# Performance work log

Hardware: AMD Instinct MI355X
Metric: run time of the kernel (lower is better)

The kernel has to match this reference:

```python
import jax, jax.numpy as jnp
import numpy as np

NEG_SLOPE = 0.2
EPS = 1e-16


def sp_gat_layer(h, src, trg, w, a_src, a_trg):
    # h: [N, f_in], w: [H, f_in, f_out], a_src/a_trg: [H, f_out]
    n = h.shape[0]
    h_prime = jnp.einsum('nf,hfo->nho', h, w)            # [N, H, O]
    attn_src = jnp.einsum('nho,ho->nh', h_prime, a_src)  # [N, H]
    attn_trg = jnp.einsum('nho,ho->nh', h_prime, a_trg)  # [N, H]
    e = jax.nn.leaky_relu(attn_src[src] + attn_trg[trg], NEG_SLOPE)  # [E, H]
    e = e - e.max()  # global max-shift, as in the torch code
    exp_e = jnp.exp(e)
    denom = jax.ops.segment_sum(exp_e, trg, num_segments=n)          # [N, H]
    neigh_attn = exp_e / (denom[trg] + EPS)                          # [E, H]
    h_weighted = h_prime[src] * neigh_attn[..., None]                # [E, H, O]
    return jax.ops.segment_sum(h_weighted, trg, num_segments=n)     # [N, H, O]


def run_stack(h, src, trg, params):
    # params: list of (w, a_src, a_trg); last layer mean over heads, others elu+flatten
    n = h.shape[0]
    n_layers = len(params)
    for i, (w, a_src, a_trg) in enumerate(params):
        out = sp_gat_layer(h, src, trg, w, a_src, a_trg)  # [N, H, O]
        if i + 1 == n_layers:
            h = out.mean(axis=1)                          # [N, O]
        else:
            h = jax.nn.elu(out.reshape(n, -1))            # [N, H*O]
    return h


def setup_inputs() -> dict:
    key = jax.random.key(0)
    ks = jax.random.split(key, 24)
    N, E = 60000, 800000
    H, F0, O = 8, 128, 32
    inp = {
        'h0': jax.random.normal(ks[0], (N, F0), jnp.float32),
        'h1': jax.random.normal(ks[1], (N, F0), jnp.float32),
        'src0': jax.random.randint(ks[2], (E,), 0, N),
        'trg0': jax.random.randint(ks[3], (E,), 0, N),
        'src1': jax.random.randint(ks[4], (E,), 0, N),
        'trg1': jax.random.randint(ks[5], (E,), 0, N),
        'w00': jax.random.normal(ks[6], (H, F0, O), jnp.float32) * 0.1,
        'asrc00': jax.random.normal(ks[7], (H, O), jnp.float32) * 0.1,
        'atrg00': jax.random.normal(ks[8], (H, O), jnp.float32) * 0.1,
        'w01': jax.random.normal(ks[9], (H, H * O, O), jnp.float32) * 0.1,
        'asrc01': jax.random.normal(ks[10], (H, O), jnp.float32) * 0.1,
        'atrg01': jax.random.normal(ks[11], (H, O), jnp.float32) * 0.1,
        'w10': jax.random.normal(ks[12], (H, F0, O), jnp.float32) * 0.1,
        'asrc10': jax.random.normal(ks[13], (H, O), jnp.float32) * 0.1,
        'atrg10': jax.random.normal(ks[14], (H, O), jnp.float32) * 0.1,
        'w11': jax.random.normal(ks[15], (H, H * O, O), jnp.float32) * 0.1,
        'asrc11': jax.random.normal(ks[16], (H, O), jnp.float32) * 0.1,
        'atrg11': jax.random.normal(ks[17], (H, O), jnp.float32) * 0.1,
        'fc_w': jax.random.normal(ks[18], (2 * O, 2), jnp.float32) * 0.1,
        'fc_b': jnp.zeros((2,), jnp.float32),
    }
    return inp


N_USER = 50000


def reference(h0, h1, src0, trg0, src1, trg1,
              w00, asrc00, atrg00, w01, asrc01, atrg01,
              w10, asrc10, atrg10, w11, asrc11, atrg11,
              fc_w, fc_b):
    emb0 = run_stack(h0, src0, trg0, [(w00, asrc00, atrg00), (w01, asrc01, atrg01)])
    emb1 = run_stack(h1, src1, trg1, [(w10, asrc10, atrg10), (w11, asrc11, atrg11)])
    ret = jnp.concatenate([emb0[:N_USER], emb1[:N_USER]], axis=-1)  # [n_user, 64]
    logits = ret @ fc_w + fc_b
    return jax.nn.log_softmax(logits, axis=-1)
```

## Files before the change

### kernel.cpp

```cpp
#include <hip/hip_runtime.h>
#include <math.h>

#define H 8
#define O 32
#define C 256
#define CAP 48
#define NEG_SLOPE 0.2f
#define EPS_V 1e-16f
#define LOG2E 1.4426950408889634f

#define W_BKT 128
#define NB_PAD 512
#define BCAP 2048
#define EPB 4096

typedef float f32x4 __attribute__((ext_vector_type(4)));
typedef float f32x2 __attribute__((ext_vector_type(2)));
typedef short bf16x8 __attribute__((ext_vector_type(8)));

__device__ __forceinline__ unsigned short f2bf(float x){
  unsigned u = __float_as_uint(x);
  unsigned r = (u + 0x7fffu + ((u >> 16) & 1u)) >> 16;
  return (unsigned short)r;
}

template<int F>
__device__ __forceinline__ void cvt_w_body(const float* __restrict__ w,
                                           short* __restrict__ wb, int t){
  constexpr int KB = F / 8;
  if (t >= 256 * KB) return;
  int c = t & 255, kb = t >> 8;
  int h = c >> 5, o = c & 31;
  bf16x8 out;
  for (int j = 0; j < 8; ++j){
    int f = kb * 8 + j;
    out[j] = (short)f2bf(w[((size_t)h * F + f) * O + o]);
  }
  *(bf16x8*)(wb + ((size_t)kb * 256 + c) * 8) = out;
}

__device__ void pass1_body(const int* __restrict__ trg, const int* __restrict__ src,
                           unsigned* __restrict__ gbuf, unsigned* __restrict__ gcur,
                           int E, int bx, int tid){
  __shared__ int cnt[NB_PAD];
  __shared__ int offl[NB_PAD];
  __shared__ unsigned baseg[NB_PAD];
  __shared__ int cur[NB_PAD];
  __shared__ unsigned payload[EPB];

  const int e0 = bx * EPB;
  const int ne = min(EPB, E - e0);
  for (int i = tid; i < NB_PAD; i += 256) cnt[i] = 0;
  __syncthreads();
  for (int i = tid; i < ne; i += 256){
    int t = trg[e0 + i];
    atomicAdd(&cnt[t >> 7], 1);
  }
  __syncthreads();
  for (int i = tid; i < NB_PAD; i += 256){
    int c = cnt[i];
    baseg[i] = c ? atomicAdd(&gcur[i], (unsigned)c) : 0u;
  }
  if (tid < 64){
    int v[8]; int s = 0;
#pragma unroll
    for (int j = 0; j < 8; ++j){ v[j] = cnt[tid * 8 + j]; s += v[j]; }
    int x = s;
#pragma unroll
    for (int d = 1; d < 64; d <<= 1){
      int o = __shfl_up(x, d, 64);
      if (tid >= d) x += o;
    }
    int base = x - s;
#pragma unroll
    for (int j = 0; j < 8; ++j){ offl[tid * 8 + j] = base; base += v[j]; }
  }
  __syncthreads();
  for (int i = tid; i < NB_PAD; i += 256) cur[i] = offl[i];
  __syncthreads();
  for (int i = tid; i < ne; i += 256){
    int t = trg[e0 + i];
    int s = src[e0 + i];
    int b = t >> 7;
    int p = atomicAdd(&cur[b], 1);
    payload[p] = ((unsigned)b << 23) | ((unsigned)(t & 127) << 16) | (unsigned)s;
  }
  __syncthreads();
  for (int i = tid; i < ne; i += 256){
    unsigned v = payload[i];
    unsigned b = v >> 23;
    unsigned pos = baseg[b] + (unsigned)(i - offl[b]);
    if (pos < BCAP) gbuf[(size_t)b * BCAP + pos] = v;
  }
}

__device__ void pass2_body(const unsigned* __restrict__ gbuf,
                           const unsigned* __restrict__ gcur,
                           unsigned short* __restrict__ csrc, int* __restrict__ degv,
                           int N, int bx, int tid){
  __shared__ unsigned short ell[W_BKT * CAP];
  __shared__ int dcnt[W_BKT];
  const int node0 = bx << 7;
  const int nn = min(W_BKT, N - node0);
  const unsigned pat = ((unsigned)N << 16) | (unsigned)N;
  unsigned* e32 = (unsigned*)ell;
  for (int i = tid; i < W_BKT * CAP / 2; i += 256) e32[i] = pat;
  for (int i = tid; i < W_BKT; i += 256) dcnt[i] = 0;
  __syncthreads();
  const int ne = min((int)gcur[bx], BCAP);
  for (int i = tid; i < ne; i += 256){
    unsigned v = gbuf[(size_t)bx * BCAP + i];
    int lt = (v >> 16) & 127;
    int p = atomicAdd(&dcnt[lt], 1);
    if (p < CAP) ell[lt * CAP + p] = (unsigned short)(v & 0xffffu);
  }
  __syncthreads();
  const uint4* s4 = (const uint4*)ell;
  uint4* d4 = (uint4*)(csrc + (size_t)node0 * CAP);
  const int n16 = nn * (CAP / 8);
  for (int i = tid; i < n16; i += 256) d4[i] = s4[i];
  for (int i = tid; i < nn; i += 256) degv[node0 + i] = dcnt[i];
}

__device__ __forceinline__ float gather_accum(
    const unsigned char* __restrict__ hp,
    const float* __restrict__ as_, float ath,
    const unsigned short* __restrict__ row, int deg, int l, int head,
    f32x2 (&acc)[4]){
  int degR = (deg + 7) & ~7;
  float dsum = 0.f;
  for (int jb = 0; jb < degR; jb += 8){
    ushort4 s4a = *(const ushort4*)(row + jb);
    ushort4 s4b = *(const ushort4*)(row + jb + 4);
    int ss[8] = {s4a.x, s4a.y, s4a.z, s4a.w, s4b.x, s4b.y, s4b.z, s4b.w};
    float xa[8];
#pragma unroll
    for (int i = 0; i < 8; ++i) xa[i] = as_[ss[i] * H + head];
    uint2 vv[8];
#pragma unroll
    for (int i = 0; i < 8; ++i)
      vv[i] = *(const uint2*)(hp + (size_t)ss[i] * C + l * 8);
#pragma unroll
    for (int i = 0; i < 8; ++i){
      float x = xa[i] + ath;
      x = fmaxf(x, NEG_SLOPE * x);
      float e = __builtin_amdgcn_exp2f(x);
      dsum += e;
      f32x2 ee = {e, e};
      f32x2 u0 = __builtin_amdgcn_cvt_pk_f32_fp8(vv[i].x, false);
      f32x2 u1 = __builtin_amdgcn_cvt_pk_f32_fp8(vv[i].x, true);
      f32x2 u2 = __builtin_amdgcn_cvt_pk_f32_fp8(vv[i].y, false);
      f32x2 u3 = __builtin_amdgcn_cvt_pk_f32_fp8(vv[i].y, true);
      acc[0] += u0 * ee;
      acc[1] += u1 * ee;
      acc[2] += u2 * ee;
      acc[3] += u3 * ee;
    }
  }
  return dsum;
}

__device__ __forceinline__ void gemm_epilogue(
    f32x4 (&acc)[2][4], int node0, int q, int m15, int wv,
    const float* __restrict__ wsv, const float* __restrict__ wtv,
    unsigned char* __restrict__ hpo, float* __restrict__ aso,
    float* __restrict__ ato, int n_nodes){
#pragma unroll
  for (int rt2 = 0; rt2 < 2; ++rt2){
    int nb = node0 + rt2 * 16 + q * 4;
    float att[4][4] = {};
#pragma unroll
    for (int ct = 0; ct < 4; ++ct){
      int col = (wv * 4 + ct) * 16 + m15;
      int hi = ct >> 1;
      int p01 = __builtin_amdgcn_cvt_pk_fp8_f32(acc[rt2][ct][0], acc[rt2][ct][1], 0, false);
      int p23 = __builtin_amdgcn_cvt_pk_fp8_f32(acc[rt2][ct][2], acc[rt2][ct][3], 0, false);
      unsigned char qb[4] = {(unsigned char)(p01 & 0xff),
                             (unsigned char)((p01 >> 8) & 0xff),
                             (unsigned char)(p23 & 0xff),
                             (unsigned char)((p23 >> 8) & 0xff)};
#pragma unroll
      for (int r = 0; r < 4; ++r){
        int n = nb + r;
        if (n < n_nodes) hpo[(size_t)n * C + col] = qb[r];
        float vr = acc[rt2][ct][r];
        att[r][hi]     = fmaf(vr, wsv[ct], att[r][hi]);
        att[r][2 + hi] = fmaf(vr, wtv[ct], att[r][2 + hi]);
      }
    }
#pragma unroll
    for (int r = 0; r < 4; ++r)
#pragma unroll
      for (int k = 0; k < 4; ++k){
        float v = att[r][k];
        v += __shfl_xor(v, 1, 64);
        v += __shfl_xor(v, 2, 64);
        v += __shfl_xor(v, 4, 64);
        v += __shfl_xor(v, 8, 64);
        att[r][k] = v;
      }
    if (m15 == 0){
      int h0i = 2 * wv;
#pragma unroll
      for (int r = 0; r < 4; ++r){
        int n = nb + r;
        if (n < n_nodes){
          aso[n * H + h0i]     = att[r][0] * LOG2E;
          aso[n * H + h0i + 1] = att[r][1] * LOG2E;
          ato[n * H + h0i]     = att[r][2] * LOG2E;
          ato[n * H + h0i + 1] = att[r][3] * LOG2E;
        }
      }
    }
  }
}

__global__ void prep_kernel(
    const float* __restrict__ w000, const float* __restrict__ w100,
    const float* __restrict__ w001, const float* __restrict__ w101,
    const int* __restrict__ t0, const int* __restrict__ t1,
    const int* __restrict__ s0, const int* __restrict__ s1,
    short* __restrict__ wb0, short* __restrict__ wb1,
    unsigned* __restrict__ gbuf, unsigned* __restrict__ gcur,
    float* __restrict__ asA, float* __restrict__ asB,
    int N, int E, int p1B, size_t wbStride, size_t asStride){
  int y = blockIdx.y;
  int bx = blockIdx.x;
  int tid = threadIdx.x;
  if (bx < 16){
    cvt_w_body<128>(y ? w100 : w000, wb0 + (size_t)y * wbStride, bx * 256 + tid);
    return;
  }
  bx -= 16;
  if (bx < 32){
    cvt_w_body<256>(y ? w101 : w001, wb1 + (size_t)y * wbStride, bx * 256 + tid);
    return;
  }
  bx -= 32;
  if (bx < p1B){
    pass1_body(y ? t1 : t0, y ? s1 : s0,
               gbuf + (size_t)y * NB_PAD * BCAP, gcur + (size_t)y * NB_PAD,
               E, bx, tid);
    return;
  }
  if (tid < H){
    asA[y * asStride + (size_t)N * H + tid] = -1e30f;
    asB[y * asStride + (size_t)N * H + tid] = -1e30f;
  }
}

__global__ __launch_bounds__(256) void binfill_gemm0_kernel(
    const unsigned* __restrict__ gbuf, const unsigned* __restrict__ gcur,
    unsigned short* __restrict__ csrc, int* __restrict__ cursor, int N, int NBk,
    const float* __restrict__ h0, const float* __restrict__ h1,
    const short* __restrict__ wb0,
    const float* __restrict__ aps0, const float* __restrict__ apt0,
    const float* __restrict__ aps1, const float* __restrict__ apt1,
    unsigned char* __restrict__ hpA, float* __restrict__ asA, float* __restrict__ atA,
    size_t wbStride, size_t hpStride, size_t asStride){
  __shared__ short atile[32 * 128];
  int y = blockIdx.y;
  int bx = blockIdx.x;
  if (bx < NBk){
    pass2_body(gbuf + (size_t)y * NB_PAD * BCAP, gcur + (size_t)y * NB_PAD,
               csrc + (size_t)y * N * CAP, cursor + (size_t)y * N, N, bx, threadIdx.x);
    return;
  }
  bx -= NBk;
  const float* hsrc = y ? h1 : h0;
  const int tid = threadIdx.x;
  const int node0 = bx * 32;
  {
    int row = tid >> 3, seg = tid & 7;
    int node = node0 + row;
    bf16x8 o0, o1;
    if (node < N){
      const float4* p4 = (const float4*)(hsrc + (size_t)node * 128 + seg * 16);
      float4 p0 = p4[0], p1 = p4[1], p2 = p4[2], p3 = p4[3];
      float v[16] = {p0.x,p0.y,p0.z,p0.w, p1.x,p1.y,p1.z,p1.w,
                     p2.x,p2.y,p2.z,p2.w, p3.x,p3.y,p3.z,p3.w};
#pragma unroll
      for (int j = 0; j < 8; ++j){ o0[j] = (short)f2bf(v[j]); o1[j] = (short)f2bf(v[8+j]); }
    } else {
#pragma unroll
      for (int j = 0; j < 8; ++j){ o0[j] = 0; o1[j] = 0; }
    }
    int key = (row & 7) << 4;
    char* base = (char*)atile + row * 256;
    *(bf16x8*)(base + ((seg * 32) ^ key))      = o0;
    *(bf16x8*)(base + ((seg * 32 + 16) ^ key)) = o1;
  }
  __syncthreads();
  const int wv = tid >> 6, lane = tid & 63;
  const int q = lane >> 4, m15 = lane & 15;
  const float* a_src = y ? aps1 : aps0;
  const float* a_trg = y ? apt1 : apt0;
  float wsv[4], wtv[4];
#pragma unroll
  for (int ct = 0; ct < 4; ++ct){
    int col = (wv * 4 + ct) * 16 + m15;
    wsv[ct] = a_src[col];
    wtv[ct] = a_trg[col];
  }
  const short* wb = wb0 + (size_t)y * wbStride;
  f32x4 acc[2][4] = {};
  const int key = (m15 & 7) << 4;
#pragma unroll
  for (int kk = 0; kk < 4; ++kk){
    const int kb0 = kk * 4 + q;
    bf16x8 a0 = *(const bf16x8*)((char*)atile + m15 * 256 + ((kb0 * 16) ^ key));
    bf16x8 a1 = *(const bf16x8*)((char*)atile + (16 + m15) * 256 + ((kb0 * 16) ^ key));
    const short* wp = wb + ((size_t)kb0 * 256 + wv * 64 + m15) * 8;
#pragma unroll
    for (int ct = 0; ct < 4; ++ct){
      bf16x8 b = *(const bf16x8*)(wp + ct * 128);
      acc[0][ct] = __builtin_amdgcn_mfma_f32_16x16x32_bf16(a0, b, acc[0][ct], 0, 0, 0);
      acc[1][ct] = __builtin_amdgcn_mfma_f32_16x16x32_bf16(a1, b, acc[1][ct], 0, 0, 0);
    }
  }
  gemm_epilogue(acc, node0, q, m15, wv, wsv, wtv,
                hpA + (size_t)y * hpStride, asA + (size_t)y * asStride,
                atA + (size_t)y * asStride, N);
}

__global__ __launch_bounds__(256, 8) void aggmm_kernel(
    const unsigned char* __restrict__ hpA,
    const float* __restrict__ asA, const float* __restrict__ atA,
    const unsigned short* __restrict__ csrc, const int* __restrict__ degv,
    const short* __restrict__ wb1,
    const float* __restrict__ aps0, const float* __restrict__ apt0,
    const float* __restrict__ aps1, const float* __restrict__ apt1,
    unsigned char* __restrict__ hpB, float* __restrict__ asB, float* __restrict__ atB,
    int N, size_t hpStride, size_t asStride, size_t wbStride){
  __shared__ short atile[32 * 256];
  const int y = blockIdx.y;
  const unsigned char* hp = hpA + (size_t)y * hpStride;
  const float* as0_ = asA + (size_t)y * asStride;
  const float* at0_ = atA + (size_t)y * asStride;
  const unsigned short* cs = csrc + (size_t)y * (size_t)N * CAP;
  const int* dg = degv + (size_t)y * N;

  const int tid = threadIdx.x;
  const int wv = tid >> 6, lane = tid & 63, half = lane >> 5, l = lane & 31;
  const int head = l >> 2;
  const int node0 = blockIdx.x * 32;

#pragma unroll
  for (int p = 0; p < 4; ++p){
    int nl = wv * 2 + half + p * 8;
    int node = node0 + nl;
    if (node < N){
      float ath = at0_[node * H + head];
      int deg = dg[node];
      deg = (deg > CAP) ? CAP : deg;
      f32x2 acc[4] = {};
      float dsum = gather_accum(hp, as0_, ath, cs + (size_t)node * CAP, deg, l, head, acc);
      float inv = __builtin_amdgcn_rcpf(dsum + EPS_V);
      bf16x8 o;
#pragma unroll
      for (int k = 0; k < 4; ++k){
        float ax = acc[k].x * inv, ay = acc[k].y * inv;
        float rx = (ax > 0.f) ? ax : (__expf(ax) - 1.f);
        float ry = (ay > 0.f) ? ay : (__expf(ay) - 1.f);
        o[2*k]   = (short)f2bf(rx);
        o[2*k+1] = (short)f2bf(ry);
      }
      *(bf16x8*)((char*)atile + nl * 512 + ((l * 16) ^ ((nl & 7) << 4))) = o;
    }
  }
  __syncthreads();

  const int q = lane >> 4, m15 = lane & 15;
  const float* a_src = y ? aps1 : aps0;
  const float* a_trg = y ? apt1 : apt0;
  float wsv[4], wtv[4];
#pragma unroll
  for (int ct = 0; ct < 4; ++ct){
    int col = (wv * 4 + ct) * 16 + m15;
    wsv[ct] = a_src[col];
    wtv[ct] = a_trg[col];
  }
  const short* wb = wb1 + (size_t)y * wbStride;
  f32x4 acc[2][4] = {};
  const int key = (m15 & 7) << 4;
#pragma unroll
  for (int kk = 0; kk < 8; ++kk){
    const int kb0 = kk * 4 + q;
    bf16x8 a0 = *(const bf16x8*)((char*)atile + m15 * 512 + ((kb0 * 16) ^ key));
    bf16x8 a1 = *(const bf16x8*)((char*)atile + (16 + m15) * 512 + ((kb0 * 16) ^ key));
    const short* wp = wb + ((size_t)kb0 * 256 + wv * 64 + m15) * 8;
#pragma unroll
    for (int ct = 0; ct < 4; ++ct){
      bf16x8 b = *(const bf16x8*)(wp + ct * 128);
      acc[0][ct] = __builtin_amdgcn_mfma_f32_16x16x32_bf16(a0, b, acc[0][ct], 0, 0, 0);
      acc[1][ct] = __builtin_amdgcn_mfma_f32_16x16x32_bf16(a1, b, acc[1][ct], 0, 0, 0);
    }
  }
  gemm_epilogue(acc, node0, q, m15, wv, wsv, wtv,
                hpB + (size_t)y * hpStride, asB + (size_t)y * asStride,
                atB + (size_t)y * asStride, N);
}

__global__ __launch_bounds__(256, 8) void gather_fc_kernel(
    const unsigned char* __restrict__ hpB, size_t hpStride,
    const float* __restrict__ asB, const float* __restrict__ atB, size_t asStride,
    const unsigned short* __restrict__ csrc, const int* __restrict__ degv, int N,
    const float* __restrict__ fw, const float* __restrict__ fb,
    float* __restrict__ out, int n_user){
  int node = (blockIdx.x * 256 + threadIdx.x) >> 6;
  if (node >= n_user) return;
  int lane = threadIdx.x & 63;
  int half = lane >> 5;
  int l = lane & 31;
  int head = l >> 2;
  const unsigned char* hps = hpB + (size_t)half * hpStride;
  const float* ass = asB + (size_t)half * asStride;
  const float* ats = atB + (size_t)half * asStride;
  const unsigned short* row = csrc + (size_t)half * N * CAP + (size_t)node * CAP;
  int deg = degv[(size_t)half * N + node];
  deg = (deg > CAP) ? CAP : deg;
  float ath = ats[node * H + head];
  f32x2 acc[4] = {};
  float dsum = gather_accum(hps, ass, ath, row, deg, l, head, acc);
  float inv = __builtin_amdgcn_rcpf(dsum + EPS_V);
#pragma unroll
  for (int k = 0; k < 4; ++k){ acc[k].x *= inv; acc[k].y *= inv; }
#pragma unroll
  for (int mask = 4; mask <= 16; mask <<= 1){
#pragma unroll
    for (int k = 0; k < 4; ++k){
      acc[k].x += __shfl_xor(acc[k].x, mask, 64);
      acc[k].y += __shfl_xor(acc[k].y, mask, 64);
    }
  }
  float p0 = 0.f, p1 = 0.f;
  if (l < 4){
    float v[8] = {acc[0].x, acc[0].y, acc[1].x, acc[1].y,
                  acc[2].x, acc[2].y, acc[3].x, acc[3].y};
#pragma unroll
    for (int j = 0; j < 8; ++j){
      float e = v[j] * 0.125f;
      int d = half * 32 + l * 8 + j;
      p0 = fmaf(e, fw[d * 2 + 0], p0);
      p1 = fmaf(e, fw[d * 2 + 1], p1);
    }
  }
#pragma unroll
  for (int mask = 1; mask <= 32; mask <<= 1){
    p0 += __shfl_xor(p0, mask, 64);
    p1 += __shfl_xor(p1, mask, 64);
  }
  if (lane == 0){
    float l0 = p0 + fb[0], l1 = p1 + fb[1];
    float m = fmaxf(l0, l1);
    float lse = m + logf(expf(l0 - m) + expf(l1 - m));
    out[(size_t)node * 2 + 0] = l0 - lse;
    out[(size_t)node * 2 + 1] = l1 - lse;
  }
}

extern "C" void kernel_launch(void* const* d_in, const int* in_sizes, int n_in,
                              void* d_out, int out_size, void* d_ws, size_t ws_size,
                              hipStream_t stream){
  const float* h0 = (const float*)d_in[0];
  const float* h1 = (const float*)d_in[1];
  const int* src0 = (const int*)d_in[2];
  const int* trg0 = (const int*)d_in[3];
  const int* src1 = (const int*)d_in[4];
  const int* trg1 = (const int*)d_in[5];
  const float* W [2][2] = {{(const float*)d_in[6],  (const float*)d_in[9]},
                           {(const float*)d_in[12], (const float*)d_in[15]}};
  const float* AS[2][2] = {{(const float*)d_in[7],  (const float*)d_in[10]},
                           {(const float*)d_in[13], (const float*)d_in[16]}};
  const float* AT[2][2] = {{(const float*)d_in[8],  (const float*)d_in[11]},
                           {(const float*)d_in[14], (const float*)d_in[17]}};
  const float* fc_w = (const float*)d_in[18];
  const float* fc_b = (const float*)d_in[19];
  float* out = (float*)d_out;

  const int N = in_sizes[0] / 128;
  const int E = in_sizes[2];
  const int n_user = out_size / 2;

  const size_t HPS = (size_t)(N + 16) * C;
  const size_t WBS = (size_t)32 * 256 * 8;
  const size_t NHP = (size_t)(N + 1) * H;

  float* ws = (float*)d_ws;
  float* attn_sA = ws;  ws += 2 * NHP;
  float* attn_tA = ws;  ws += 2 * NHP;
  float* attn_sB = ws;  ws += 2 * NHP;
  float* attn_tB = ws;  ws += 2 * NHP;
  unsigned char* hpA = (unsigned char*)ws;  ws += 2 * HPS / 4;
  unsigned char* hpB = (unsigned char*)ws;  ws += 2 * HPS / 4;
  short* wb0 = (short*)ws;  ws += 2 * WBS / 2;
  short* wb1 = (short*)ws;  ws += 2 * WBS / 2;
  unsigned short* csrc = (unsigned short*)ws;  ws += (size_t)2 * N * CAP / 2;
  int* cursor = (int*)ws;  ws += (size_t)2 * N;
  unsigned* gbuf = (unsigned*)ws;  ws += (size_t)2 * NB_PAD * BCAP;
  unsigned* gcur = (unsigned*)ws;  ws += 2 * NB_PAD;

  const int gemm_grid = (N + 31) / 32;
  const int NBk = (N + W_BKT - 1) / W_BKT;
  const int p1B = (E + EPB - 1) / EPB;
  const int gFC = (n_user * 64 + 255) / 256;

  hipMemsetAsync(gcur, 0, (size_t)2 * NB_PAD * sizeof(unsigned), stream);
  prep_kernel<<<dim3(16 + 32 + p1B + 1, 2), 256, 0, stream>>>(
      W[0][0], W[1][0], W[0][1], W[1][1],
      trg0, trg1, src0, src1,
      wb0, wb1, gbuf, gcur, attn_sA, attn_sB,
      N, E, p1B, WBS, NHP);
  binfill_gemm0_kernel<<<dim3(NBk + gemm_grid, 2), 256, 0, stream>>>(
      gbuf, gcur, csrc, cursor, N, NBk,
      h0, h1, wb0, AS[0][0], AT[0][0], AS[1][0], AT[1][0],
      hpA, attn_sA, attn_tA, WBS, HPS, NHP);
  aggmm_kernel<<<dim3(gemm_grid, 2), 256, 0, stream>>>(
      hpA, attn_sA, attn_tA, csrc, cursor, wb1,
      AS[0][1], AT[0][1], AS[1][1], AT[1][1],
      hpB, attn_sB, attn_tB, N, HPS, NHP, WBS);
  gather_fc_kernel<<<gFC, 256, 0, stream>>>(
      hpB, HPS, attn_sB, attn_tB, NHP, csrc, cursor, N, fc_w, fc_b, out, n_user);
}
```

Baseline: 355.9 us.

## Fold attention vectors into weights and compute logits via extra MFMA; dynamic node queue

Precomputes W·a_src and W·a_trg per head in the prep kernel, so attention logits come from one extra MFMA column tile per GEMM instead of per-element FMAs plus cross-lane shuffle reductions in the epilogue. Separately, the aggregation phase of aggmm now hands out nodes through a shared-memory atomic counter instead of a fixed 4-node-per-wave assignment, to balance uneven degrees. The cost is bf16 rounding of the folded weights, which changes the numerics of the logits, plus shared atomics and a serialized loop.

```diff
diff --git a/kernel.cpp b/kernel.cpp
--- a/kernel.cpp
+++ b/kernel.cpp
@@ -37,6 +37,21 @@
     out[j] = (short)f2bf(w[((size_t)h * F + f) * O + o]);
   }
   *(bf16x8*)(wb + ((size_t)kb * 256 + c) * 8) = out;
+}
+
+template<int F>
+__device__ __forceinline__ void cvt_wa_body(const float* __restrict__ w,
+                                            const float* __restrict__ as,
+                                            const float* __restrict__ at,
+                                            short* __restrict__ wa, int t){
+  if (t >= F * 16) return;
+  int k = t >> 4, e = t & 15, h = e >> 1;
+  const float* a = (e & 1) ? at : as;
+  float s = 0.f;
+#pragma unroll
+  for (int o = 0; o < O; ++o)
+    s = fmaf(w[((size_t)h * F + k) * O + o], a[h * O + o], s);
+  wa[((size_t)(k >> 3) * 16 + e) * 8 + (k & 7)] = (short)f2bf(s * LOG2E);
 }
 
 __device__ void pass1_body(const int* __restrict__ trg, const int* __restrict__ src,
@@ -160,19 +175,15 @@
   return dsum;
 }
 
-__device__ __forceinline__ void gemm_epilogue(
+__device__ __forceinline__ void hp_store_epilogue(
     f32x4 (&acc)[2][4], int node0, int q, int m15, int wv,
-    const float* __restrict__ wsv, const float* __restrict__ wtv,
-    unsigned char* __restrict__ hpo, float* __restrict__ aso,
-    float* __restrict__ ato, int n_nodes){
+    unsigned char* __restrict__ hpo, int n_nodes){
 #pragma unroll
   for (int rt2 = 0; rt2 < 2; ++rt2){
     int nb = node0 + rt2 * 16 + q * 4;
-    float att[4][4] = {};
 #pragma unroll
     for (int ct = 0; ct < 4; ++ct){
       int col = (wv * 4 + ct) * 16 + m15;
-      int hi = ct >> 1;
       int p01 = __builtin_amdgcn_cvt_pk_fp8_f32(acc[rt2][ct][0], acc[rt2][ct][1], 0, false);
       int p23 = __builtin_amdgcn_cvt_pk_fp8_f32(acc[rt2][ct][2], acc[rt2][ct][3], 0, false);
       unsigned char qb[4] = {(unsigned char)(p01 & 0xff),
@@ -183,34 +194,23 @@
       for (int r = 0; r < 4; ++r){
         int n = nb + r;
         if (n < n_nodes) hpo[(size_t)n * C + col] = qb[r];
-        float vr = acc[rt2][ct][r];
-        att[r][hi]     = fmaf(vr, wsv[ct], att[r][hi]);
-        att[r][2 + hi] = fmaf(vr, wtv[ct], att[r][2 + hi]);
       }
     }
-#pragma unroll
-    for (int r = 0; r < 4; ++r)
-#pragma unroll
-      for (int k = 0; k < 4; ++k){
-        float v = att[r][k];
-        v += __shfl_xor(v, 1, 64);
-        v += __shfl_xor(v, 2, 64);
-        v += __shfl_xor(v, 4, 64);
-        v += __shfl_xor(v, 8, 64);
-        att[r][k] = v;
-      }
-    if (m15 == 0){
-      int h0i = 2 * wv;
-#pragma unroll
-      for (int r = 0; r < 4; ++r){
-        int n = nb + r;
-        if (n < n_nodes){
-          aso[n * H + h0i]     = att[r][0] * LOG2E;
-          aso[n * H + h0i + 1] = att[r][1] * LOG2E;
-          ato[n * H + h0i]     = att[r][2] * LOG2E;
-          ato[n * H + h0i + 1] = att[r][3] * LOG2E;
-        }
-      }
+  }
+}
+
+__device__ __forceinline__ void logit_store(
+    f32x4 (&acce)[2], int node0, int q, int m15,
+    float* __restrict__ aso, float* __restrict__ ato, int n_nodes){
+  int head = m15 >> 1;
+  float* dst = (m15 & 1) ? ato : aso;
+#pragma unroll
+  for (int rt2 = 0; rt2 < 2; ++rt2){
+    int nb = node0 + rt2 * 16 + q * 4;
+#pragma unroll
+    for (int r = 0; r < 4; ++r){
+      int n = nb + r;
+      if (n < n_nodes) dst[n * H + head] = acce[rt2][r];
     }
   }
 }
@@ -218,9 +218,14 @@
 __global__ void prep_kernel(
     const float* __restrict__ w000, const float* __restrict__ w100,
     const float* __restrict__ w001, const float* __restrict__ w101,
+    const float* __restrict__ as00, const float* __restrict__ as10,
+    const float* __restrict__ as01, const float* __restrict__ as11,
+    const float* __restrict__ at00, const float* __restrict__ at10,
+    const float* __restrict__ at01, const float* __restrict__ at11,
     const int* __restrict__ t0, const int* __restrict__ t1,
     const int* __restrict__ s0, const int* __restrict__ s1,
     short* __restrict__ wb0, short* __restrict__ wb1,
+    short* __restrict__ wa0, short* __restrict__ wa1,
     unsigned* __restrict__ gbuf, unsigned* __restrict__ gcur,
     float* __restrict__ asA, float* __restrict__ asB,
     int N, int E, int p1B, size_t wbStride, size_t asStride){
@@ -237,6 +242,18 @@
     return;
   }
   bx -= 32;
+  if (bx < 8){
+    cvt_wa_body<128>(y ? w100 : w000, y ? as10 : as00, y ? at10 : at00,
+                     wa0 + (size_t)y * 2048, bx * 256 + tid);
+    return;
+  }
+  bx -= 8;
+  if (bx < 16){
+    cvt_wa_body<256>(y ? w101 : w001, y ? as11 : as01, y ? at11 : at01,
+                     wa1 + (size_t)y * 4096, bx * 256 + tid);
+    return;
+  }
+  bx -= 16;
   if (bx < p1B){
     pass1_body(y ? t1 : t0, y ? s1 : s0,
                gbuf + (size_t)y * NB_PAD * BCAP, gcur + (size_t)y * NB_PAD,
@@ -253,9 +270,7 @@
     const unsigned* __restrict__ gbuf, const unsigned* __restrict__ gcur,
     unsigned short* __restrict__ csrc, int* __restrict__ cursor, int N, int NBk,
     const float* __restrict__ h0, const float* __restrict__ h1,
-    const short* __restrict__ wb0,
-    const float* __restrict__ aps0, const float* __restrict__ apt0,
-    const float* __restrict__ aps1, const float* __restrict__ apt1,
+    const short* __restrict__ wb0, const short* __restrict__ wa0,
     unsigned char* __restrict__ hpA, float* __restrict__ asA, float* __restrict__ atA,
     size_t wbStride, size_t hpStride, size_t asStride){
   __shared__ short atile[32 * 128];
@@ -293,17 +308,10 @@
   __syncthreads();
   const int wv = tid >> 6, lane = tid & 63;
   const int q = lane >> 4, m15 = lane & 15;
-  const float* a_src = y ? aps1 : aps0;
-  const float* a_trg = y ? apt1 : apt0;
-  float wsv[4], wtv[4];
-#pragma unroll
-  for (int ct = 0; ct < 4; ++ct){
-    int col = (wv * 4 + ct) * 16 + m15;
-    wsv[ct] = a_src[col];
-    wtv[ct] = a_trg[col];
-  }
   const short* wb = wb0 + (size_t)y * wbStride;
+  const short* wa = wa0 + (size_t)y * 2048;
   f32x4 acc[2][4] = {};
+  f32x4 acce[2] = {};
   const int key = (m15 & 7) << 4;
 #pragma unroll
   for (int kk = 0; kk < 4; ++kk){
@@ -317,22 +325,27 @@
       acc[0][ct] = __builtin_amdgcn_mfma_f32_16x16x32_bf16(a0, b, acc[0][ct], 0, 0, 0);
       acc[1][ct] = __builtin_amdgcn_mfma_f32_16x16x32_bf16(a1, b, acc[1][ct], 0, 0, 0);
     }
-  }
-  gemm_epilogue(acc, node0, q, m15, wv, wsv, wtv,
-                hpA + (size_t)y * hpStride, asA + (size_t)y * asStride,
-                atA + (size_t)y * asStride, N);
+    if (wv == 0){
+      bf16x8 ba = *(const bf16x8*)(wa + ((size_t)kb0 * 16 + m15) * 8);
+      acce[0] = __builtin_amdgcn_mfma_f32_16x16x32_bf16(a0, ba, acce[0], 0, 0, 0);
+      acce[1] = __builtin_amdgcn_mfma_f32_16x16x32_bf16(a1, ba, acce[1], 0, 0, 0);
+    }
+  }
+  hp_store_epilogue(acc, node0, q, m15, wv, hpA + (size_t)y * hpStride, N);
+  if (wv == 0)
+    logit_store(acce, node0, q, m15,
+                asA + (size_t)y * asStride, atA + (size_t)y * asStride, N);
 }
 
 __global__ __launch_bounds__(256, 8) void aggmm_kernel(
     const unsigned char* __restrict__ hpA,
     const float* __restrict__ asA, const float* __restrict__ atA,
     const unsigned short* __restrict__ csrc, const int* __restrict__ degv,
-    const short* __restrict__ wb1,
-    const float* __restrict__ aps0, const float* __restrict__ apt0,
-    const float* __restrict__ aps1, const float* __restrict__ apt1,
+    const short* __restrict__ wb1, const short* __restrict__ wa1,
     unsigned char* __restrict__ hpB, float* __restrict__ asB, float* __restrict__ atB,
     int N, size_t hpStride, size_t asStride, size_t wbStride){
   __shared__ short atile[32 * 256];
+  __shared__ int qcur;
   const int y = blockIdx.y;
   const unsigned char* hp = hpA + (size_t)y * hpStride;
   const float* as0_ = asA + (size_t)y * asStride;
@@ -345,9 +358,13 @@
   const int head = l >> 2;
   const int node0 = blockIdx.x * 32;
 
-#pragma unroll
-  for (int p = 0; p < 4; ++p){
-    int nl = wv * 2 + half + p * 8;
+  if (tid == 0) qcur = 0;
+  __syncthreads();
+  for (;;){
+    int p = 0;
+    if (l == 0) p = atomicAdd(&qcur, 1);
+    int nl = __shfl(p, half << 5, 64);
+    if (nl >= 32) break;
     int node = node0 + nl;
     if (node < N){
       float ath = at0_[node * H + head];
@@ -371,17 +388,10 @@
   __syncthreads();
 
   const int q = lane >> 4, m15 = lane & 15;
-  const float* a_src = y ? aps1 : aps0;
-  const float* a_trg = y ? apt1 : apt0;
-  float wsv[4], wtv[4];
-#pragma unroll
-  for (int ct = 0; ct < 4; ++ct){
-    int col = (wv * 4 + ct) * 16 + m15;
-    wsv[ct] = a_src[col];
-    wtv[ct] = a_trg[col];
-  }
   const short* wb = wb1 + (size_t)y * wbStride;
+  const short* wa = wa1 + (size_t)y * 4096;
   f32x4 acc[2][4] = {};
+  f32x4 acce[2] = {};
   const int key = (m15 & 7) << 4;
 #pragma unroll
   for (int kk = 0; kk < 8; ++kk){
@@ -395,10 +405,16 @@
       acc[0][ct] = __builtin_amdgcn_mfma_f32_16x16x32_bf16(a0, b, acc[0][ct], 0, 0, 0);
       acc[1][ct] = __builtin_amdgcn_mfma_f32_16x16x32_bf16(a1, b, acc[1][ct], 0, 0, 0);
     }
-  }
-  gemm_epilogue(acc, node0, q, m15, wv, wsv, wtv,
-                hpB + (size_t)y * hpStride, asB + (size_t)y * asStride,
-                atB + (size_t)y * asStride, N);
+    if (wv == 0){
+      bf16x8 ba = *(const bf16x8*)(wa + ((size_t)kb0 * 16 + m15) * 8);
+      acce[0] = __builtin_amdgcn_mfma_f32_16x16x32_bf16(a0, ba, acce[0], 0, 0, 0);
+      acce[1] = __builtin_amdgcn_mfma_f32_16x16x32_bf16(a1, ba, acce[1], 0, 0, 0);
+    }
+  }
+  hp_store_epilogue(acc, node0, q, m15, wv, hpB + (size_t)y * hpStride, N);
+  if (wv == 0)
+    logit_store(acce, node0, q, m15,
+                asB + (size_t)y * asStride, atB + (size_t)y * asStride, N);
 }
 
 __global__ __launch_bounds__(256, 8) void gather_fc_kernel(
@@ -495,6 +511,8 @@
   unsigned char* hpB = (unsigned char*)ws;  ws += 2 * HPS / 4;
   short* wb0 = (short*)ws;  ws += 2 * WBS / 2;
   short* wb1 = (short*)ws;  ws += 2 * WBS / 2;
+  short* wa0 = (short*)ws;  ws += 2 * 2048 / 2;
+  short* wa1 = (short*)ws;  ws += 2 * 4096 / 2;
   unsigned short* csrc = (unsigned short*)ws;  ws += (size_t)2 * N * CAP / 2;
   int* cursor = (int*)ws;  ws += (size_t)2 * N;
   unsigned* gbuf = (unsigned*)ws;  ws += (size_t)2 * NB_PAD * BCAP;
@@ -506,18 +524,18 @@
   const int gFC = (n_user * 64 + 255) / 256;
 
   hipMemsetAsync(gcur, 0, (size_t)2 * NB_PAD * sizeof(unsigned), stream);
-  prep_kernel<<<dim3(16 + 32 + p1B + 1, 2), 256, 0, stream>>>(
+  prep_kernel<<<dim3(16 + 32 + 8 + 16 + p1B + 1, 2), 256, 0, stream>>>(
       W[0][0], W[1][0], W[0][1], W[1][1],
+      AS[0][0], AS[1][0], AS[0][1], AS[1][1],
+      AT[0][0], AT[1][0], AT[0][1], AT[1][1],
       trg0, trg1, src0, src1,
-      wb0, wb1, gbuf, gcur, attn_sA, attn_sB,
+      wb0, wb1, wa0, wa1, gbuf, gcur, attn_sA, attn_sB,
       N, E, p1B, WBS, NHP);
   binfill_gemm0_kernel<<<dim3(NBk + gemm_grid, 2), 256, 0, stream>>>(
       gbuf, gcur, csrc, cursor, N, NBk,
-      h0, h1, wb0, AS[0][0], AT[0][0], AS[1][0], AT[1][0],
-      hpA, attn_sA, attn_tA, WBS, HPS, NHP);
+      h0, h1, wb0, wa0, hpA, attn_sA, attn_tA, WBS, HPS, NHP);
   aggmm_kernel<<<dim3(gemm_grid, 2), 256, 0, stream>>>(
-      hpA, attn_sA, attn_tA, csrc, cursor, wb1,
-      AS[0][1], AT[0][1], AS[1][1], AT[1][1],
+      hpA, attn_sA, attn_tA, csrc, cursor, wb1, wa1,
       hpB, attn_sB, attn_tB, N, HPS, NHP, WBS);
   gather_fc_kernel<<<gFC, 256, 0, stream>>>(
       hpB, HPS, attn_sB, attn_tB, NHP, csrc, cursor, N, fc_w, fc_b, out, n_user);
```

New measurement: 343.9 us (median of 2 runs). 1.03x faster.
